# Kernel optimization log

Hardware: AMD Instinct MI355X
Metric: run time of the kernel (lower is better)

Reference implementation:

```python
import jax, jax.numpy as jnp
import numpy as np

P = 2048
D = 1024
H = 16
DH = D // H
HID = 32


def setup_inputs() -> dict:
    key = jax.random.key(0)
    ks = jax.random.split(key, 10)
    s = 0.02
    return {
        "x": jax.random.normal(ks[0], (P, D), jnp.float32),
        "rel": jax.random.normal(ks[1], (P, P, 2), jnp.float32),
        "w_qkv": jax.random.normal(ks[2], (D, 3 * D), jnp.float32) * s,
        "w_proj": jax.random.normal(ks[3], (D, D), jnp.float32) * s,
        "rpb_w1": jax.random.normal(ks[4], (2, HID), jnp.float32) * s,
        "rpb_b1": jnp.zeros((HID,), jnp.float32),
        "rpb_w2": jax.random.normal(ks[5], (HID, HID), jnp.float32) * s,
        "rpb_b2": jnp.zeros((HID,), jnp.float32),
        "rpb_w3": jax.random.normal(ks[6], (HID, 1), jnp.float32) * s,
        "rpb_b3": jnp.zeros((1,), jnp.float32),
    }


def reference(x, rel, w_qkv, w_proj, rpb_w1, rpb_b1, rpb_w2, rpb_b2, rpb_w3, rpb_b3):
    scale = 1.0 / np.sqrt(DH)
    qkv = x @ w_qkv                                   # [P, 3D]
    q, k, v = jnp.split(qkv, 3, axis=-1)
    # [P, D] -> [H, P, DH]
    q = q.reshape(P, H, DH).transpose(1, 0, 2)
    k = k.reshape(P, H, DH).transpose(1, 0, 2)
    v = v.reshape(P, H, DH).transpose(1, 0, 2)
    logits = jnp.einsum('hpd,hqd->hpq', q, k) * scale  # [H, P, P]
    # RelPosBias MLP: (dx,dy) -> scalar, applied over [P, P, 2]
    hcur = jax.nn.relu(rel @ rpb_w1 + rpb_b1)
    hcur = jax.nn.relu(hcur @ rpb_w2 + rpb_b2)
    bias = (hcur @ rpb_w3 + rpb_b3)[..., 0]            # [P, P]
    logits = logits + bias[None]
    attn = jax.nn.softmax(logits, axis=-1)
    out = jnp.einsum('hpq,hqd->hpd', attn, v)          # [H, P, DH]
    out = out.transpose(1, 0, 2).reshape(P, D)
    return out @ w_proj
```

## Files before the change

### kernel.cpp

```cpp
#include <hip/hip_runtime.h>
#include <hip/hip_bf16.h>
#include <type_traits>

typedef __attribute__((ext_vector_type(8))) short bf16x8;
typedef __attribute__((ext_vector_type(4))) float floatx4;
typedef __attribute__((ext_vector_type(2))) float float2v;

__device__ __forceinline__ float bf2f(unsigned short u) {
    union { unsigned int x; float f; } v; v.x = ((unsigned int)u) << 16; return v.f;
}
__device__ __forceinline__ unsigned short f2bf(float f) {
    union { float f; unsigned int u; } v; v.f = f;
    unsigned int x = v.u;
    unsigned int r = x + 0x7fffu + ((x >> 16) & 1u);
    return (unsigned short)(r >> 16);
}

typedef const __attribute__((address_space(1))) unsigned int u32_g;
typedef __attribute__((address_space(3))) unsigned int u32_l;
__device__ __forceinline__ void gld_lds16(const void* g, void* l) {
    __builtin_amdgcn_global_load_lds((u32_g*)g, (u32_l*)l, 16, 0, 0);
}

__device__ __forceinline__ void trans32(const float* __restrict__ in,
                                        unsigned short* __restrict__ out,
                                        int K, int N, int bx, int by,
                                        unsigned short (*T)[33]) {
    const int n0 = bx * 32, k0 = by * 32;
    const int r = threadIdx.x >> 3;
    const int c4 = (threadIdx.x & 7) * 4;
    float4 v = *reinterpret_cast<const float4*>(in + (size_t)(k0 + r) * N + n0 + c4);
    T[c4 + 0][r] = f2bf(v.x);
    T[c4 + 1][r] = f2bf(v.y);
    T[c4 + 2][r] = f2bf(v.z);
    T[c4 + 3][r] = f2bf(v.w);
    __syncthreads();
    ushort4 o = {T[r][c4], T[r][c4 + 1], T[r][c4 + 2], T[r][c4 + 3]};
    *reinterpret_cast<ushort4*>(out + (size_t)(n0 + r) * K + k0 + c4) = o;
}

__global__ __launch_bounds__(256) void prep(const float* __restrict__ x,
                                            unsigned short* __restrict__ xb,
                                            const float* __restrict__ wq,
                                            unsigned short* __restrict__ wqT,
                                            const float* __restrict__ wp,
                                            unsigned short* __restrict__ wpT) {
    __shared__ unsigned short T[32][33];
    const int b = blockIdx.x;
    if (b < 1024) {
        size_t i = ((size_t)b * 256 + threadIdx.x) * 8;
        float4 a = *reinterpret_cast<const float4*>(x + i);
        float4 c = *reinterpret_cast<const float4*>(x + i + 4);
        unsigned short t[8] = {f2bf(a.x), f2bf(a.y), f2bf(a.z), f2bf(a.w),
                               f2bf(c.x), f2bf(c.y), f2bf(c.z), f2bf(c.w)};
        *reinterpret_cast<uint4*>(xb + i) = *reinterpret_cast<const uint4*>(t);
    } else if (b < 4096) {
        int t = b - 1024;
        trans32(wq, wqT, 1024, 3072, t % 96, t / 96, T);
    } else {
        int t = b - 4096;
        trans32(wp, wpT, 1024, 1024, t % 32, t / 32, T);
    }
}

template<int BN, typename TC>
__global__ __launch_bounds__(256) void gemm_abt(const unsigned short* __restrict__ A,
                                                const unsigned short* __restrict__ Bt,
                                                TC* __restrict__ C,
                                                int M, int N, int K) {
    constexpr int NT = BN / 32;
    __shared__ __align__(16) unsigned short As[64 * 32];
    __shared__ __align__(16) unsigned short Bs[BN * 32];

    const int tid = threadIdx.x;
    const int wave = tid >> 6;
    const int lane = tid & 63;
    const int m15 = lane & 15;
    const int quad = lane >> 4;
    const int wm = wave >> 1;
    const int wn = wave & 1;
    const int m0 = blockIdx.y * 64;
    const int n0 = blockIdx.x * BN;

    const int srow = lane >> 2;
    const int scol = (lane & 3) * 8;

    floatx4 acc[2][NT];
#pragma unroll
    for (int mt = 0; mt < 2; mt++)
#pragma unroll
        for (int nt = 0; nt < NT; nt++) acc[mt][nt] = {0.f, 0.f, 0.f, 0.f};

    for (int k0 = 0; k0 < K; k0 += 32) {
        gld_lds16(A + (size_t)(m0 + wave * 16 + srow) * K + k0 + scol, &As[wave * 16 * 32]);
#pragma unroll
        for (int i = 0; i < BN / 64; i++) {
            int j = wave * (BN / 64) + i;
            gld_lds16(Bt + (size_t)(n0 + j * 16 + srow) * K + k0 + scol, &Bs[j * 16 * 32]);
        }
        __syncthreads();

        bf16x8 a[2];
#pragma unroll
        for (int mt = 0; mt < 2; mt++)
            a[mt] = *reinterpret_cast<bf16x8*>(&As[(wm * 32 + mt * 16 + m15) * 32 + quad * 8]);
#pragma unroll
        for (int nt = 0; nt < NT; nt++) {
            bf16x8 b = *reinterpret_cast<bf16x8*>(&Bs[(wn * (BN / 2) + nt * 16 + m15) * 32 + quad * 8]);
#pragma unroll
            for (int mt = 0; mt < 2; mt++)
                acc[mt][nt] = __builtin_amdgcn_mfma_f32_16x16x32_bf16(a[mt], b, acc[mt][nt], 0, 0, 0);
        }
        __syncthreads();
    }

#pragma unroll
    for (int mt = 0; mt < 2; mt++)
#pragma unroll
        for (int nt = 0; nt < NT; nt++)
#pragma unroll
            for (int i = 0; i < 4; i++) {
                int row = m0 + wm * 32 + mt * 16 + quad * 4 + i;
                int col = n0 + wn * (BN / 2) + nt * 16 + m15;
                if constexpr (std::is_same<TC, float>::value)
                    C[(size_t)row * N + col] = acc[mt][nt][i];
                else
                    C[(size_t)row * N + col] = f2bf(acc[mt][nt][i]);
            }
}

__global__ __launch_bounds__(256) void rpb_mfma_kernel(const float* __restrict__ rel,
                                                       const float* __restrict__ w1,
                                                       const float* __restrict__ b1,
                                                       const float* __restrict__ w2,
                                                       const float* __restrict__ b2,
                                                       const float* __restrict__ w3,
                                                       const float* __restrict__ b3,
                                                       unsigned short* __restrict__ biasb) {
    __shared__ __align__(16) unsigned short Ah[4][64 * 40];

    const int tid = threadIdx.x;
    const int wave = tid >> 6;
    const int lane = tid & 63;
    const int m15 = lane & 15;
    const int quad = lane >> 4;

    float2v w1a2[16], w1b2[16], b12[16];
#pragma unroll
    for (int cp = 0; cp < 16; cp++) {
        w1a2[cp] = {w1[2 * cp], w1[2 * cp + 1]};
        w1b2[cp] = {w1[32 + 2 * cp], w1[32 + 2 * cp + 1]};
        b12[cp]  = {b1[2 * cp], b1[2 * cp + 1]};
    }

    bf16x8 bf0, bf1;
    {
        unsigned short t0[8], t1[8];
#pragma unroll
        for (int j = 0; j < 8; j++) {
            int k = quad * 8 + j;
            t0[j] = f2bf(w2[k * 32 + m15]);
            t1[j] = f2bf(w2[k * 32 + 16 + m15]);
        }
        bf0 = *reinterpret_cast<bf16x8*>(t0);
        bf1 = *reinterpret_cast<bf16x8*>(t1);
    }
    const float b2a = b2[m15], b2b = b2[16 + m15];
    const float2v w3a2 = {w3[m15], w3[m15]};
    const float2v w3b2 = {w3[16 + m15], w3[16 + m15]};
    const float b3v = b3[0];
    const float LOG2E = 1.44269504f;
    const float2v z2 = {0.f, 0.f};

    unsigned short* myA = Ah[wave];
    const int base = blockIdx.x * 1024 + wave * 64;

    for (int it = 0; it < 4; ++it) {
        const int pix0 = base + it * 256;
        float2 dxy = *reinterpret_cast<const float2*>(rel + (size_t)(pix0 + lane) * 2);
        float2v dx2 = {dxy.x, dxy.x}, dy2 = {dxy.y, dxy.y};

        unsigned int hp[16];
#pragma unroll
        for (int cp = 0; cp < 16; cp++) {
            float2v h = __builtin_elementwise_fma(dx2, w1a2[cp],
                         __builtin_elementwise_fma(dy2, w1b2[cp], b12[cp]));
            h = __builtin_elementwise_max(h, z2);
            hp[cp] = __builtin_amdgcn_perm(__float_as_uint(h.y), __float_as_uint(h.x), 0x07060302u);
        }
#pragma unroll
        for (int ch = 0; ch < 4; ch++)
            *reinterpret_cast<uint4*>(&myA[lane * 40 + ch * 8]) = *reinterpret_cast<const uint4*>(&hp[ch * 4]);

#pragma unroll
        for (int t = 0; t < 4; t++) {
            bf16x8 a = *reinterpret_cast<bf16x8*>(&myA[(t * 16 + m15) * 40 + quad * 8]);
            floatx4 d0 = {b2a, b2a, b2a, b2a};
            floatx4 d1 = {b2b, b2b, b2b, b2b};
            d0 = __builtin_amdgcn_mfma_f32_16x16x32_bf16(a, bf0, d0, 0, 0, 0);
            d1 = __builtin_amdgcn_mfma_f32_16x16x32_bf16(a, bf1, d1, 0, 0, 0);

            float2v p0 = __builtin_elementwise_max(__builtin_shufflevector(d0, d0, 0, 1), z2);
            float2v p1 = __builtin_elementwise_max(__builtin_shufflevector(d0, d0, 2, 3), z2);
            float2v q0 = __builtin_elementwise_max(__builtin_shufflevector(d1, d1, 0, 1), z2);
            float2v q1 = __builtin_elementwise_max(__builtin_shufflevector(d1, d1, 2, 3), z2);
            float2v s01 = __builtin_elementwise_fma(q0, w3b2, p0 * w3a2);
            float2v s23 = __builtin_elementwise_fma(q1, w3b2, p1 * w3a2);
            float s[4] = {s01.x, s01.y, s23.x, s23.y};

#pragma unroll
            for (int i = 0; i < 4; i++) {
                int iv;
                iv = __builtin_amdgcn_update_dpp(__float_as_int(s[i]), __float_as_int(s[i]), 0x121, 0xf, 0xf, false);
                s[i] += __int_as_float(iv);
                iv = __builtin_amdgcn_update_dpp(__float_as_int(s[i]), __float_as_int(s[i]), 0x122, 0xf, 0xf, false);
                s[i] += __int_as_float(iv);
                iv = __builtin_amdgcn_update_dpp(__float_as_int(s[i]), __float_as_int(s[i]), 0x124, 0xf, 0xf, false);
                s[i] += __int_as_float(iv);
                iv = __builtin_amdgcn_update_dpp(__float_as_int(s[i]), __float_as_int(s[i]), 0x128, 0xf, 0xf, false);
                s[i] += __int_as_float(iv);
            }
            if (m15 == 0) {
                unsigned short o[4];
#pragma unroll
                for (int i = 0; i < 4; i++) o[i] = f2bf((s[i] + b3v) * LOG2E);
                *reinterpret_cast<ushort4*>(biasb + (size_t)pix0 + t * 16 + quad * 4) =
                    *reinterpret_cast<const ushort4*>(o);
            }
        }
    }
}

__global__ __launch_bounds__(512, 4) void attn_kernel(const unsigned short* __restrict__ qkv,
                                                      const unsigned short* __restrict__ biasb,
                                                      unsigned short* __restrict__ attn_out) {
    const int h = blockIdx.x;
    const int q0 = blockIdx.y * 64;
    __shared__ __align__(16) unsigned short Kst[2][64 * 72];
    __shared__ __align__(16) unsigned short Vst[2][64 * 72];
    __shared__ __align__(16) unsigned short Ps[8][16 * 72];

    const int tid = threadIdx.x;
    const int g = tid >> 8;
    const int w = (tid >> 6) & 3;
    const int lane = tid & 63;
    const int ltid = tid & 255;
    const int m15 = lane & 15;
    const int quad = lane >> 4;

    bf16x8 qf[2];
#pragma unroll
    for (int kh = 0; kh < 2; kh++)
        qf[kh] = *reinterpret_cast<const bf16x8*>(
            qkv + (size_t)(q0 + w * 16 + m15) * 3072 + h * 64 + kh * 32 + quad * 8);

    const int kr0 = ltid >> 3, kd0 = (ltid & 7) * 8;
    const int ka = (ltid & 31) * 2;
    const int vd0 = (ltid >> 5) * 8;

    unsigned short* Kc = Kst[g];
    unsigned short* Vc = Vst[g];
    const size_t kofs = (size_t)g * 1024;

    uint4 kreg0 = *reinterpret_cast<const uint4*>(qkv + (kofs + kr0) * 3072 + 1024 + h * 64 + kd0);
    uint4 kreg1 = *reinterpret_cast<const uint4*>(qkv + (kofs + kr0 + 32) * 3072 + 1024 + h * 64 + kd0);
    uint4 vrega = *reinterpret_cast<const uint4*>(qkv + (kofs + ka) * 3072 + 2048 + h * 64 + vd0);
    uint4 vregb = *reinterpret_cast<const uint4*>(qkv + (kofs + ka + 1) * 3072 + 2048 + h * 64 + vd0);
    unsigned short br[16];
#pragma unroll
    for (int nt = 0; nt < 4; nt++)
#pragma unroll
        for (int i = 0; i < 4; i++)
            br[nt * 4 + i] = biasb[(size_t)(q0 + w * 16 + quad * 4 + i) * 2048 + kofs + nt * 16 + m15];

    float rs[4] = {0.f, 0.f, 0.f, 0.f};
    floatx4 acc[4];
#pragma unroll
    for (int i = 0; i < 4; i++) acc[i] = {0.f, 0.f, 0.f, 0.f};
    const float c1 = 0.125f * 1.44269504f;

    for (int kt = 0; kt < 16; ++kt) {
        __syncthreads();

        *reinterpret_cast<uint4*>(&Kc[kr0 * 72 + kd0]) = kreg0;
        *reinterpret_cast<uint4*>(&Kc[(kr0 + 32) * 72 + kd0]) = kreg1;
        {
            const unsigned int* aw = reinterpret_cast<const unsigned int*>(&vrega);
            const unsigned int* bw = reinterpret_cast<const unsigned int*>(&vregb);
#pragma unroll
            for (int wd = 0; wd < 4; wd++) {
                unsigned int lo = __builtin_amdgcn_perm(bw[wd], aw[wd], 0x05040100u);
                unsigned int hi = __builtin_amdgcn_perm(bw[wd], aw[wd], 0x07060302u);
                *reinterpret_cast<unsigned int*>(&Vc[(vd0 + 2 * wd) * 72 + ka]) = lo;
                *reinterpret_cast<unsigned int*>(&Vc[(vd0 + 2 * wd + 1) * 72 + ka]) = hi;
            }
        }
        __syncthreads();

        if (kt < 15) {
            const size_t kb = kofs + (size_t)(kt + 1) * 64;
            kreg0 = *reinterpret_cast<const uint4*>(qkv + (kb + kr0) * 3072 + 1024 + h * 64 + kd0);
            kreg1 = *reinterpret_cast<const uint4*>(qkv + (kb + kr0 + 32) * 3072 + 1024 + h * 64 + kd0);
            vrega = *reinterpret_cast<const uint4*>(qkv + (kb + ka) * 3072 + 2048 + h * 64 + vd0);
            vregb = *reinterpret_cast<const uint4*>(qkv + (kb + ka + 1) * 3072 + 2048 + h * 64 + vd0);
        }

        floatx4 s[4];
#pragma unroll
        for (int nt = 0; nt < 4; nt++) s[nt] = {0.f, 0.f, 0.f, 0.f};
#pragma unroll
        for (int kh = 0; kh < 2; kh++) {
#pragma unroll
            for (int nt = 0; nt < 4; nt++) {
                bf16x8 b = *reinterpret_cast<bf16x8*>(&Kc[(nt * 16 + m15) * 72 + kh * 32 + quad * 8]);
                s[nt] = __builtin_amdgcn_mfma_f32_16x16x32_bf16(qf[kh], b, s[nt], 0, 0, 0);
            }
        }

        float p[4][4];
#pragma unroll
        for (int nt = 0; nt < 4; nt++)
#pragma unroll
            for (int i = 0; i < 4; i++) {
                float lg = fmaf(s[nt][i], c1, bf2f(br[nt * 4 + i]));
                p[nt][i] = __builtin_amdgcn_exp2f(lg);
                rs[i] += p[nt][i];
            }

        if (kt < 15) {
            const size_t kb = kofs + (size_t)(kt + 1) * 64;
#pragma unroll
            for (int nt = 0; nt < 4; nt++)
#pragma unroll
                for (int i = 0; i < 4; i++)
                    br[nt * 4 + i] = biasb[(size_t)(q0 + w * 16 + quad * 4 + i) * 2048 + kb + nt * 16 + m15];
        }

        unsigned short* Pw = Ps[tid >> 6];
#pragma unroll
        for (int nt = 0; nt < 4; nt++)
#pragma unroll
            for (int i = 0; i < 4; i++)
                Pw[(quad * 4 + i) * 72 + nt * 16 + m15] = f2bf(p[nt][i]);
        __asm__ volatile("s_waitcnt lgkmcnt(0)" ::: "memory");

#pragma unroll
        for (int kh = 0; kh < 2; kh++) {
            bf16x8 a = *reinterpret_cast<bf16x8*>(&Pw[m15 * 72 + kh * 32 + quad * 8]);
#pragma unroll
            for (int nt = 0; nt < 4; nt++) {
                bf16x8 b = *reinterpret_cast<bf16x8*>(&Vc[(nt * 16 + m15) * 72 + kh * 32 + quad * 8]);
                acc[nt] = __builtin_amdgcn_mfma_f32_16x16x32_bf16(a, b, acc[nt], 0, 0, 0);
            }
        }
    }

    float rsum[4];
#pragma unroll
    for (int i = 0; i < 4; i++) {
        float r = rs[i];
        r += __shfl_xor(r, 1);
        r += __shfl_xor(r, 2);
        r += __shfl_xor(r, 4);
        r += __shfl_xor(r, 8);
        rsum[i] = r;
    }

    float* accbuf = reinterpret_cast<float*>(&Kst[0][0]);
    float* lbuf = accbuf + 4096;

    __syncthreads();
    if (g == 1) {
#pragma unroll
        for (int nt = 0; nt < 4; nt++)
#pragma unroll
            for (int i = 0; i < 4; i++)
                accbuf[(w * 16 + quad * 4 + i) * 64 + nt * 16 + m15] = acc[nt][i];
        if (m15 == 0) {
#pragma unroll
            for (int i = 0; i < 4; i++) lbuf[w * 16 + quad * 4 + i] = rsum[i];
        }
    }
    __syncthreads();
    if (g == 0) {
        float linv[4];
#pragma unroll
        for (int i = 0; i < 4; i++)
            linv[i] = 1.f / (rsum[i] + lbuf[w * 16 + quad * 4 + i]);
#pragma unroll
        for (int nt = 0; nt < 4; nt++)
#pragma unroll
            for (int i = 0; i < 4; i++) {
                float o = (acc[nt][i] + accbuf[(w * 16 + quad * 4 + i) * 64 + nt * 16 + m15]) * linv[i];
                int row = q0 + w * 16 + quad * 4 + i;
                int col = h * 64 + nt * 16 + m15;
                attn_out[(size_t)row * 1024 + col] = f2bf(o);
            }
    }
}

extern "C" void kernel_launch(void* const* d_in, const int* in_sizes, int n_in,
                              void* d_out, int out_size, void* d_ws, size_t ws_size,
                              hipStream_t stream) {
    const float* x      = (const float*)d_in[0];
    const float* rel    = (const float*)d_in[1];
    const float* w_qkv  = (const float*)d_in[2];
    const float* w_proj = (const float*)d_in[3];
    const float* w1     = (const float*)d_in[4];
    const float* b1     = (const float*)d_in[5];
    const float* w2     = (const float*)d_in[6];
    const float* b2     = (const float*)d_in[7];
    const float* w3     = (const float*)d_in[8];
    const float* b3     = (const float*)d_in[9];

    char* ws = (char*)d_ws;
    unsigned short* qkv   = (unsigned short*)ws;
    unsigned short* biasb = (unsigned short*)(ws + 12582912);
    unsigned short* xb    = (unsigned short*)(ws + 20971520);
    unsigned short* attn  = xb;
    unsigned short* wqT   = (unsigned short*)(ws + 25165824);
    unsigned short* wpT   = (unsigned short*)(ws + 31457280);
    float* out = (float*)d_out;

    prep<<<5120, 256, 0, stream>>>(x, xb, w_qkv, wqT, w_proj, wpT);
    gemm_abt<128, unsigned short><<<dim3(24, 32), 256, 0, stream>>>(xb, wqT, qkv, 2048, 3072, 1024);
    rpb_mfma_kernel<<<4096, 256, 0, stream>>>(rel, w1, b1, w2, b2, w3, b3, biasb);
    attn_kernel<<<dim3(16, 32), 512, 0, stream>>>(qkv, biasb, attn);
    gemm_abt<64, float><<<dim3(16, 32), 256, 0, stream>>>(attn, wpT, out, 2048, 1024, 1024);
}
```

Measured before the change: 233.6 us.

## Transpose RPB MLP MFMA so hidden features lie on K lanes, drop LDS staging

Swaps the MFMA operand roles in the relative-position-bias MLP so W2 is the A operand and hidden activations are built directly in registers as the B operand. Each lane computes only its 8 of the 32 first-layer features for one pixel, so the LDS round trip and the per-lane 32-feature computation go away. The final reduction becomes two cross-quad shuffles instead of four DPP steps per output, and LOG2E is folded into w3 and b3. In exchange, each lane now loads rel redundantly across quads and writes narrow 2-byte stores gated by quad==t.

```diff
diff --git a/kernel.cpp b/kernel.cpp
--- a/kernel.cpp
+++ b/kernel.cpp
@@ -137,23 +137,13 @@
                                                        const float* __restrict__ w3,
                                                        const float* __restrict__ b3,
                                                        unsigned short* __restrict__ biasb) {
-    __shared__ __align__(16) unsigned short Ah[4][64 * 40];
-
     const int tid = threadIdx.x;
     const int wave = tid >> 6;
     const int lane = tid & 63;
     const int m15 = lane & 15;
     const int quad = lane >> 4;
 
-    float2v w1a2[16], w1b2[16], b12[16];
-#pragma unroll
-    for (int cp = 0; cp < 16; cp++) {
-        w1a2[cp] = {w1[2 * cp], w1[2 * cp + 1]};
-        w1b2[cp] = {w1[32 + 2 * cp], w1[32 + 2 * cp + 1]};
-        b12[cp]  = {b1[2 * cp], b1[2 * cp + 1]};
-    }
-
-    bf16x8 bf0, bf1;
+    bf16x8 af0, af1;
     {
         unsigned short t0[8], t1[8];
 #pragma unroll
@@ -162,71 +152,76 @@
             t0[j] = f2bf(w2[k * 32 + m15]);
             t1[j] = f2bf(w2[k * 32 + 16 + m15]);
         }
-        bf0 = *reinterpret_cast<bf16x8*>(t0);
-        bf1 = *reinterpret_cast<bf16x8*>(t1);
-    }
-    const float b2a = b2[m15], b2b = b2[16 + m15];
-    const float2v w3a2 = {w3[m15], w3[m15]};
-    const float2v w3b2 = {w3[16 + m15], w3[16 + m15]};
-    const float b3v = b3[0];
+        af0 = *reinterpret_cast<bf16x8*>(t0);
+        af1 = *reinterpret_cast<bf16x8*>(t1);
+    }
+
+    float2v w1a2[4], w1b2[4], b12[4];
+#pragma unroll
+    for (int p = 0; p < 4; p++) {
+        int base = quad * 8 + 2 * p;
+        w1a2[p] = {w1[base], w1[base + 1]};
+        w1b2[p] = {w1[32 + base], w1[32 + base + 1]};
+        b12[p]  = {b1[base], b1[base + 1]};
+    }
+
+    floatx4 b2r0, b2r1;
+    float2v w3p00, w3p01, w3p10, w3p11;
     const float LOG2E = 1.44269504f;
+    {
+        float4 t0 = *reinterpret_cast<const float4*>(b2 + quad * 4);
+        float4 t1 = *reinterpret_cast<const float4*>(b2 + 16 + quad * 4);
+        b2r0 = {t0.x, t0.y, t0.z, t0.w};
+        b2r1 = {t1.x, t1.y, t1.z, t1.w};
+        float4 u0 = *reinterpret_cast<const float4*>(w3 + quad * 4);
+        float4 u1 = *reinterpret_cast<const float4*>(w3 + 16 + quad * 4);
+        w3p00 = {u0.x * LOG2E, u0.y * LOG2E};
+        w3p01 = {u0.z * LOG2E, u0.w * LOG2E};
+        w3p10 = {u1.x * LOG2E, u1.y * LOG2E};
+        w3p11 = {u1.z * LOG2E, u1.w * LOG2E};
+    }
+    const float b3s = b3[0] * LOG2E;
     const float2v z2 = {0.f, 0.f};
 
-    unsigned short* myA = Ah[wave];
     const int base = blockIdx.x * 1024 + wave * 64;
 
     for (int it = 0; it < 4; ++it) {
         const int pix0 = base + it * 256;
-        float2 dxy = *reinterpret_cast<const float2*>(rel + (size_t)(pix0 + lane) * 2);
-        float2v dx2 = {dxy.x, dxy.x}, dy2 = {dxy.y, dxy.y};
-
-        unsigned int hp[16];
-#pragma unroll
-        for (int cp = 0; cp < 16; cp++) {
-            float2v h = __builtin_elementwise_fma(dx2, w1a2[cp],
-                         __builtin_elementwise_fma(dy2, w1b2[cp], b12[cp]));
-            h = __builtin_elementwise_max(h, z2);
-            hp[cp] = __builtin_amdgcn_perm(__float_as_uint(h.y), __float_as_uint(h.x), 0x07060302u);
-        }
-#pragma unroll
-        for (int ch = 0; ch < 4; ch++)
-            *reinterpret_cast<uint4*>(&myA[lane * 40 + ch * 8]) = *reinterpret_cast<const uint4*>(&hp[ch * 4]);
-
 #pragma unroll
         for (int t = 0; t < 4; t++) {
-            bf16x8 a = *reinterpret_cast<bf16x8*>(&myA[(t * 16 + m15) * 40 + quad * 8]);
-            floatx4 d0 = {b2a, b2a, b2a, b2a};
-            floatx4 d1 = {b2b, b2b, b2b, b2b};
-            d0 = __builtin_amdgcn_mfma_f32_16x16x32_bf16(a, bf0, d0, 0, 0, 0);
-            d1 = __builtin_amdgcn_mfma_f32_16x16x32_bf16(a, bf1, d1, 0, 0, 0);
-
-            float2v p0 = __builtin_elementwise_max(__builtin_shufflevector(d0, d0, 0, 1), z2);
-            float2v p1 = __builtin_elementwise_max(__builtin_shufflevector(d0, d0, 2, 3), z2);
-            float2v q0 = __builtin_elementwise_max(__builtin_shufflevector(d1, d1, 0, 1), z2);
-            float2v q1 = __builtin_elementwise_max(__builtin_shufflevector(d1, d1, 2, 3), z2);
-            float2v s01 = __builtin_elementwise_fma(q0, w3b2, p0 * w3a2);
-            float2v s23 = __builtin_elementwise_fma(q1, w3b2, p1 * w3a2);
-            float s[4] = {s01.x, s01.y, s23.x, s23.y};
-
-#pragma unroll
-            for (int i = 0; i < 4; i++) {
-                int iv;
-                iv = __builtin_amdgcn_update_dpp(__float_as_int(s[i]), __float_as_int(s[i]), 0x121, 0xf, 0xf, false);
-                s[i] += __int_as_float(iv);
-                iv = __builtin_amdgcn_update_dpp(__float_as_int(s[i]), __float_as_int(s[i]), 0x122, 0xf, 0xf, false);
-                s[i] += __int_as_float(iv);
-                iv = __builtin_amdgcn_update_dpp(__float_as_int(s[i]), __float_as_int(s[i]), 0x124, 0xf, 0xf, false);
-                s[i] += __int_as_float(iv);
-                iv = __builtin_amdgcn_update_dpp(__float_as_int(s[i]), __float_as_int(s[i]), 0x128, 0xf, 0xf, false);
-                s[i] += __int_as_float(iv);
-            }
-            if (m15 == 0) {
-                unsigned short o[4];
-#pragma unroll
-                for (int i = 0; i < 4; i++) o[i] = f2bf((s[i] + b3v) * LOG2E);
-                *reinterpret_cast<ushort4*>(biasb + (size_t)pix0 + t * 16 + quad * 4) =
-                    *reinterpret_cast<const ushort4*>(o);
-            }
+            const int px = pix0 + t * 16;
+            float2 dxy = *reinterpret_cast<const float2*>(rel + (size_t)(px + m15) * 2);
+            float2v dx2 = {dxy.x, dxy.x}, dy2 = {dxy.y, dxy.y};
+
+            unsigned int hp[4];
+#pragma unroll
+            for (int p = 0; p < 4; p++) {
+                float2v h = __builtin_elementwise_fma(dx2, w1a2[p],
+                             __builtin_elementwise_fma(dy2, w1b2[p], b12[p]));
+                h = __builtin_elementwise_max(h, z2);
+                hp[p] = __builtin_amdgcn_perm(__float_as_uint(h.y), __float_as_uint(h.x), 0x07060302u);
+            }
+            bf16x8 hb = *reinterpret_cast<bf16x8*>(hp);
+
+            floatx4 d0 = __builtin_amdgcn_mfma_f32_16x16x32_bf16(af0, hb, b2r0, 0, 0, 0);
+            floatx4 d1 = __builtin_amdgcn_mfma_f32_16x16x32_bf16(af1, hb, b2r1, 0, 0, 0);
+
+            float2v m00 = __builtin_elementwise_max(__builtin_shufflevector(d0, d0, 0, 1), z2);
+            float2v m01 = __builtin_elementwise_max(__builtin_shufflevector(d0, d0, 2, 3), z2);
+            float2v m10 = __builtin_elementwise_max(__builtin_shufflevector(d1, d1, 0, 1), z2);
+            float2v m11 = __builtin_elementwise_max(__builtin_shufflevector(d1, d1, 2, 3), z2);
+            float2v acc2 = m00 * w3p00;
+            acc2 = __builtin_elementwise_fma(m01, w3p01, acc2);
+            acc2 = __builtin_elementwise_fma(m10, w3p10, acc2);
+            acc2 = __builtin_elementwise_fma(m11, w3p11, acc2);
+            float s = acc2.x + acc2.y;
+
+            s += __shfl_xor(s, 16);
+            s += __shfl_xor(s, 32);
+            s += b3s;
+
+            if (quad == t)
+                biasb[(size_t)px + m15] = f2bf(s);
         }
     }
 }
```

Result: no change. 230.6 us (-1.3%).
